# Kernel tuning notes

Hardware: AMD Instinct MI355X
Metric: run time of the kernel (lower is better)

The kernel has to match this reference:

```python
import jax, jax.numpy as jnp
import numpy as np

B, S, D = 8, 2048, 1024
E, K = 16, 2
H = 4096
SD, SH = D // E, H // E  # 64, 256
MAX_SEQ = 2048


def setup_inputs() -> dict:
    key = jax.random.key(0)
    ks = jax.random.split(key, 5)
    x = jax.random.normal(ks[0], (B, S, D), dtype=jnp.float32)
    w_switch = jax.random.normal(ks[1], (D * MAX_SEQ, E), dtype=jnp.float32) * 0.001
    b_switch = jnp.zeros((E,), dtype=jnp.float32)
    w1 = jax.random.normal(ks[2], (E, SD, SH), dtype=jnp.float32) * (1.0 / np.sqrt(SD))
    b1 = jnp.zeros((E, SH), dtype=jnp.float32)
    w2 = jax.random.normal(ks[3], (H, D), dtype=jnp.float32) * (1.0 / np.sqrt(H))
    b2 = jnp.zeros((D,), dtype=jnp.float32)
    return {"x": x, "w_switch": w_switch, "b_switch": b_switch,
            "w1": w1, "b1": b1, "w2": w2, "b2": b2}


def reference(x, w_switch, b_switch, w1, b1, w2, b2):
    # Router: softmax over experts from flattened first MAX_SEQ tokens
    x0 = x[:, :MAX_SEQ].reshape(B, -1)                      # [B, D*MAX_SEQ]
    route_prob = jax.nn.softmax(x0 @ w_switch + b_switch)   # [B, E]
    # Top-k expert membership mask per batch element
    _, topk_idx = jax.lax.top_k(route_prob, K)              # [B, K]
    mask = jax.nn.one_hot(topk_idx, E, dtype=x.dtype).sum(axis=1)  # [B, E]
    # Per-expert linear on the expert's channel slice, masked combine
    xe = x.reshape(B, S, E, SD)                              # [B, S, E, SD]
    h = jnp.einsum('bsed,edh->bseh', xe, w1) + b1            # [B, S, E, SH]
    h = h * mask[:, None, :, None]                           # zero out non-routed
    out = h.reshape(B, S, H)                                 # [B, S, H]
    out = jax.nn.gelu(out, approximate=False)                # exact GELU (torch default)
    return out @ w2 + b2                                     # [B, S, D]
```

## Files before the change

kernel.cpp:

```cpp
#include <hip/hip_runtime.h>
#include <hip/hip_bf16.h>

#define B_  8
#define S_  2048
#define D_  1024
#define E_  16
#define SD_ 64
#define SH_ 256
#define H_  4096
#define R_  (D_ * S_)
#define NBLK_ 2048

typedef __attribute__((ext_vector_type(8))) short bf16x8;
typedef __attribute__((ext_vector_type(4))) float f32x4;

static __device__ __forceinline__ short f2bf(float f) {
    union { float f; unsigned u; } v; v.f = f;
    unsigned r = v.u + 0x7fffu + ((v.u >> 16) & 1u);
    return (short)(r >> 16);
}

__global__ void convert_w(const float* __restrict__ w1, const float* __restrict__ w2,
                          short* __restrict__ w1f, short* __restrict__ w2f) {
    int blk = blockIdx.x;
    if (blk < 128) {
        int t = blk * 256 + threadIdx.x;
        int lane = t & 63, ntile = (t >> 6) & 15, ks = (t >> 10) & 1, e = t >> 11;
        int k0 = ks * 32 + ((lane >> 4) << 3);
        int n  = (ntile << 4) + (lane & 15);
        const float* src = w1 + ((size_t)(e * 64 + k0) * 256 + n);
        bf16x8 o;
        #pragma unroll
        for (int j = 0; j < 8; ++j) o[j] = f2bf(src[(size_t)j * 256]);
        *(bf16x8*)(w1f + ((size_t)t << 3)) = o;
    } else {
        int t = (blk - 128) * 256 + threadIdx.x;
        int lane = t & 63, ntile = (t >> 6) & 63, kg = t >> 12;
        int k0 = (kg << 5) + ((lane >> 4) << 3);
        int n  = (ntile << 4) + (lane & 15);
        const float* src = w2 + ((size_t)k0 * 1024 + n);
        bf16x8 o;
        #pragma unroll
        for (int j = 0; j < 8; ++j) o[j] = f2bf(src[(size_t)j * 1024]);
        *(bf16x8*)(w2f + ((size_t)t << 3)) = o;
    }
}

__global__ __launch_bounds__(256, 4) void router_kernel(const float* __restrict__ x,
                                                        const float* __restrict__ wsw,
                                                        float* __restrict__ partials) {
    __shared__ float red[512];
    int tid = threadIdx.x;
    int wid = tid >> 6, lane = tid & 63;
    int q = lane & 3, rsub = lane >> 2;
    int gw = (blockIdx.x << 2) + wid;
    size_t rowbase = (size_t)gw << 8;
    const float4* w4 = (const float4*)wsw;

    float acc[8][4];
    #pragma unroll
    for (int b = 0; b < 8; ++b)
        #pragma unroll
        for (int j = 0; j < 4; ++j) acc[b][j] = 0.f;

    #pragma unroll 4
    for (int it = 0; it < 16; ++it) {
        size_t row0 = rowbase + (size_t)(it << 4);
        float4 w = w4[row0 * 4 + lane];
        size_t xrow = row0 + rsub;
        float xv[8];
        #pragma unroll
        for (int b = 0; b < 8; ++b) xv[b] = x[(size_t)b * R_ + xrow];
        #pragma unroll
        for (int b = 0; b < 8; ++b) {
            acc[b][0] = fmaf(xv[b], w.x, acc[b][0]);
            acc[b][1] = fmaf(xv[b], w.y, acc[b][1]);
            acc[b][2] = fmaf(xv[b], w.z, acc[b][2]);
            acc[b][3] = fmaf(xv[b], w.w, acc[b][3]);
        }
    }

    #pragma unroll
    for (int b = 0; b < 8; ++b)
        #pragma unroll
        for (int j = 0; j < 4; ++j) {
            float v = acc[b][j];
            v += __shfl_xor(v, 4);
            v += __shfl_xor(v, 8);
            v += __shfl_xor(v, 16);
            v += __shfl_xor(v, 32);
            acc[b][j] = v;
        }

    if (lane < 4) {
        #pragma unroll
        for (int b = 0; b < 8; ++b)
            #pragma unroll
            for (int j = 0; j < 4; ++j)
                red[(wid << 7) + b * 16 + q * 4 + j] = acc[b][j];
    }
    __syncthreads();
    if (tid < 128)
        partials[(size_t)tid * NBLK_ + blockIdx.x] =
            red[tid] + red[128 + tid] + red[256 + tid] + red[384 + tid];
}

__global__ __launch_bounds__(256) void reduce_kernel(const float* __restrict__ partials,
                                                     float* __restrict__ logits) {
    __shared__ float s[256];
    int e = blockIdx.x, tid = threadIdx.x;
    const float4* p4 = (const float4*)(partials + (size_t)e * NBLK_);
    float t = 0.f;
    #pragma unroll
    for (int i = 0; i < 2; ++i) {
        float4 v = p4[i * 256 + tid];
        t += v.x + v.y + v.z + v.w;
    }
    s[tid] = t;
    __syncthreads();
    #pragma unroll
    for (int off = 128; off; off >>= 1) {
        if (tid < off) s[tid] += s[tid + off];
        __syncthreads();
    }
    if (tid == 0) logits[e] = s[0];
}

__global__ void topk_kernel(const float* __restrict__ logits,
                            const float* __restrict__ bsw,
                            int* __restrict__ experts) {
    int b = threadIdx.x;
    if (b >= 8) return;
    float v[16];
    #pragma unroll
    for (int e = 0; e < 16; ++e) v[e] = logits[b * 16 + e] + bsw[e];
    int i0 = 0; float m0 = v[0];
    #pragma unroll
    for (int e = 1; e < 16; ++e) if (v[e] > m0) { m0 = v[e]; i0 = e; }
    int i1 = -1; float m1 = -3.4e38f;
    #pragma unroll
    for (int e = 0; e < 16; ++e) if (e != i0 && v[e] > m1) { m1 = v[e]; i1 = e; }
    experts[2 * b]     = i0;
    experts[2 * b + 1] = i1;
}

__global__ __launch_bounds__(256, 2) void mlp_kernel(
        const float* __restrict__ x, const int* __restrict__ experts,
        const short* __restrict__ w1f, const float* __restrict__ b1,
        const short* __restrict__ w2f, const float* __restrict__ b2,
        float* __restrict__ out) {
    __shared__ short G[32][520];

    int blk  = blockIdx.x;
    int b    = blk & 7;
    int tok0 = (blk >> 3) << 5;
    int e0 = experts[2 * b], e1 = experts[2 * b + 1];
    int tid = threadIdx.x;
    int wid = tid >> 6, lane = tid & 63;
    int slot  = wid >> 1;
    int ex    = slot ? e1 : e0;
    int nhalf = wid & 1;
    int lrow = lane & 15, lk8 = (lane >> 4) << 3;

    f32x4 acc1[2][8];
    #pragma unroll
    for (int m = 0; m < 2; ++m)
        #pragma unroll
        for (int n = 0; n < 8; ++n) acc1[m][n] = (f32x4){0.f, 0.f, 0.f, 0.f};

    #pragma unroll
    for (int ks = 0; ks < 2; ++ks) {
        bf16x8 a[2];
        #pragma unroll
        for (int m = 0; m < 2; ++m) {
            const float* xp = x + (((size_t)b * S_ + tok0 + m * 16 + lrow) * D_
                                   + ex * 64 + ks * 32 + lk8);
            float4 f0 = *(const float4*)xp;
            float4 f1 = *(const float4*)(xp + 4);
            bf16x8 av;
            av[0] = f2bf(f0.x); av[1] = f2bf(f0.y); av[2] = f2bf(f0.z); av[3] = f2bf(f0.w);
            av[4] = f2bf(f1.x); av[5] = f2bf(f1.y); av[6] = f2bf(f1.z); av[7] = f2bf(f1.w);
            a[m] = av;
        }
        #pragma unroll
        for (int nt = 0; nt < 8; ++nt) {
            int ntg = nhalf * 8 + nt;
            bf16x8 bf = *(const bf16x8*)(w1f + ((((size_t)(ex * 2 + ks) * 16 + ntg) * 64 + lane) << 3));
            acc1[0][nt] = __builtin_amdgcn_mfma_f32_16x16x32_bf16(a[0], bf, acc1[0][nt], 0, 0, 0);
            acc1[1][nt] = __builtin_amdgcn_mfma_f32_16x16x32_bf16(a[1], bf, acc1[1][nt], 0, 0, 0);
        }
    }

    #pragma unroll
    for (int nt = 0; nt < 8; ++nt) {
        int ncol = (nhalf * 8 + nt) * 16 + lrow;
        float bb = b1[ex * 256 + ncol];
        #pragma unroll
        for (int m = 0; m < 2; ++m) {
            int r0 = m * 16 + ((lane >> 4) << 2);
            #pragma unroll
            for (int r = 0; r < 4; ++r) {
                float v = acc1[m][nt][r] + bb;
                v = 0.5f * v * (1.0f + erff(v * 0.70710678118f));
                G[r0 + r][slot * 256 + ncol] = f2bf(v);
            }
        }
    }
    __syncthreads();

    f32x4 acc2[2][16];
    #pragma unroll
    for (int m = 0; m < 2; ++m)
        #pragma unroll
        for (int n = 0; n < 16; ++n) acc2[m][n] = (f32x4){0.f, 0.f, 0.f, 0.f};

    for (int ks = 0; ks < 16; ++ks) {
        int e  = (ks < 8) ? e0 : e1;
        int kg = e * 8 + (ks & 7);
        bf16x8 a0 = *(const bf16x8*)&G[lrow][ks * 32 + lk8];
        bf16x8 a1 = *(const bf16x8*)&G[16 + lrow][ks * 32 + lk8];
        #pragma unroll
        for (int nt = 0; nt < 16; ++nt) {
            int ntg = wid * 16 + nt;
            bf16x8 bf = *(const bf16x8*)(w2f + ((((size_t)kg * 64 + ntg) * 64 + lane) << 3));
            acc2[0][nt] = __builtin_amdgcn_mfma_f32_16x16x32_bf16(a0, bf, acc2[0][nt], 0, 0, 0);
            acc2[1][nt] = __builtin_amdgcn_mfma_f32_16x16x32_bf16(a1, bf, acc2[1][nt], 0, 0, 0);
        }
    }

    size_t obase = ((size_t)b * S_ + tok0) * D_;
    #pragma unroll
    for (int nt = 0; nt < 16; ++nt) {
        int d = wid * 256 + nt * 16 + lrow;
        float bb = b2[d];
        #pragma unroll
        for (int m = 0; m < 2; ++m) {
            int r0 = m * 16 + ((lane >> 4) << 2);
            #pragma unroll
            for (int r = 0; r < 4; ++r)
                out[obase + (size_t)(r0 + r) * D_ + d] = acc2[m][nt][r] + bb;
        }
    }
}

extern "C" void kernel_launch(void* const* d_in, const int* in_sizes, int n_in,
                              void* d_out, int out_size, void* d_ws, size_t ws_size,
                              hipStream_t stream) {
    const float* x   = (const float*)d_in[0];
    const float* wsw = (const float*)d_in[1];
    const float* bsw = (const float*)d_in[2];
    const float* w1  = (const float*)d_in[3];
    const float* b1  = (const float*)d_in[4];
    const float* w2  = (const float*)d_in[5];
    const float* b2  = (const float*)d_in[6];
    float* out = (float*)d_out;

    int*   experts  = (int*)d_ws;
    float* logits   = (float*)((char*)d_ws + 512);
    float* partials = (float*)((char*)d_ws + 4096);
    short* w1f = (short*)((char*)d_ws + 4096 + 1048576);
    short* w2f = (short*)((char*)d_ws + 4096 + 1048576 + 524288);

    router_kernel<<<NBLK_, 256, 0, stream>>>(x, wsw, partials);
    reduce_kernel<<<128, 256, 0, stream>>>(partials, logits);
    topk_kernel<<<1, 64, 0, stream>>>(logits, bsw, experts);
    convert_w<<<2176, 256, 0, stream>>>(w1, w2, w1f, w2f);
    mlp_kernel<<<512, 256, 0, stream>>>(x, experts, w1f, b1, w2f, b2, out);
}
```

Baseline: 124.6 us.

## Remap router lanes to batch-by-row and broadcast weights via shuffles

The router GEMV now assigns each lane a batch index and a pair of adjacent rows. x is read as float2 per lane instead of eight scattered scalar loads per lane, and each thread keeps 16 expert accumulators. Weight rows are still loaded once per wave as float4 and broadcast to the lanes that need them through __shfl. This should make the x loads contiguous and cut the reduction shuffles from four levels to three. The cost is 16 shuffles per row pair added to the inner loop.

```diff
diff --git a/kernel.cpp b/kernel.cpp
--- a/kernel.cpp
+++ b/kernel.cpp
@@ -52,52 +52,54 @@
     __shared__ float red[512];
     int tid = threadIdx.x;
     int wid = tid >> 6, lane = tid & 63;
-    int q = lane & 3, rsub = lane >> 2;
+    int b = lane & 7, rh = lane >> 3;
     int gw = (blockIdx.x << 2) + wid;
     size_t rowbase = (size_t)gw << 8;
     const float4* w4 = (const float4*)wsw;
-
-    float acc[8][4];
-    #pragma unroll
-    for (int b = 0; b < 8; ++b)
-        #pragma unroll
-        for (int j = 0; j < 4; ++j) acc[b][j] = 0.f;
-
-    #pragma unroll 4
+    const float2* x2 = (const float2*)(x + (size_t)b * R_ + rowbase) + rh;
+
+    float acc[16];
+    #pragma unroll
+    for (int e = 0; e < 16; ++e) acc[e] = 0.f;
+
+    int sbase = rh << 3;
+
+    #pragma unroll 2
     for (int it = 0; it < 16; ++it) {
-        size_t row0 = rowbase + (size_t)(it << 4);
-        float4 w = w4[row0 * 4 + lane];
-        size_t xrow = row0 + rsub;
-        float xv[8];
-        #pragma unroll
-        for (int b = 0; b < 8; ++b) xv[b] = x[(size_t)b * R_ + xrow];
-        #pragma unroll
-        for (int b = 0; b < 8; ++b) {
-            acc[b][0] = fmaf(xv[b], w.x, acc[b][0]);
-            acc[b][1] = fmaf(xv[b], w.y, acc[b][1]);
-            acc[b][2] = fmaf(xv[b], w.z, acc[b][2]);
-            acc[b][3] = fmaf(xv[b], w.w, acc[b][3]);
-        }
-    }
-
-    #pragma unroll
-    for (int b = 0; b < 8; ++b)
-        #pragma unroll
-        for (int j = 0; j < 4; ++j) {
-            float v = acc[b][j];
-            v += __shfl_xor(v, 4);
-            v += __shfl_xor(v, 8);
-            v += __shfl_xor(v, 16);
-            v += __shfl_xor(v, 32);
-            acc[b][j] = v;
-        }
-
-    if (lane < 4) {
-        #pragma unroll
-        for (int b = 0; b < 8; ++b)
+        float2 xv = x2[it << 3];
+        float4 wA = w4[((rowbase + ((size_t)it << 4)) << 2) + lane];
+
+        #pragma unroll
+        for (int rr = 0; rr < 2; ++rr) {
+            float xs = rr ? xv.y : xv.x;
             #pragma unroll
-            for (int j = 0; j < 4; ++j)
-                red[(wid << 7) + b * 16 + q * 4 + j] = acc[b][j];
+            for (int eq = 0; eq < 4; ++eq) {
+                int s = sbase + (rr << 2) + eq;
+                float w0 = __shfl(wA.x, s);
+                float w1 = __shfl(wA.y, s);
+                float w2v = __shfl(wA.z, s);
+                float w3 = __shfl(wA.w, s);
+                acc[eq * 4 + 0] = fmaf(xs, w0, acc[eq * 4 + 0]);
+                acc[eq * 4 + 1] = fmaf(xs, w1, acc[eq * 4 + 1]);
+                acc[eq * 4 + 2] = fmaf(xs, w2v, acc[eq * 4 + 2]);
+                acc[eq * 4 + 3] = fmaf(xs, w3, acc[eq * 4 + 3]);
+            }
+        }
+    }
+
+    #pragma unroll
+    for (int e = 0; e < 16; ++e) {
+        float v = acc[e];
+        v += __shfl_xor(v, 8);
+        v += __shfl_xor(v, 16);
+        v += __shfl_xor(v, 32);
+        acc[e] = v;
+    }
+
+    if (lane < 8) {
+        #pragma unroll
+        for (int e = 0; e < 16; ++e)
+            red[(wid << 7) + b * 16 + e] = acc[e];
     }
     __syncthreads();
     if (tid < 128)
```

Result: slower. 127.3 us (+2.2%).

## Double-buffer router loads into LDS via async global_load_lds

Applied to the files above, without the earlier changes.

Rewrites the router GEMV so that each block covers 2048 rows in 16 chunks of 128. Each chunk's router weights and x values are staged into double-buffered shared memory with direct global-to-LDS loads, so the next chunk's loads overlap the current chunk's FMAs. The block count is halved, which shrinks the partials buffer, simplifies the reduce kernel and moves the workspace offsets. The intent is better memory coalescing and latency hiding for the bandwidth-bound router. In exchange the kernel adds a barrier per chunk, uses more LDS and runs fewer blocks.

```diff
diff --git a/kernel.cpp b/kernel.cpp
--- a/kernel.cpp
+++ b/kernel.cpp
@@ -9,7 +9,10 @@
 #define SH_ 256
 #define H_  4096
 #define R_  (D_ * S_)
-#define NBLK_ 2048
+#define NBLK_ 1024
+#define RT_ROWS 2048
+#define RT_CHUNK 128
+#define RT_NCHUNK 16
 
 typedef __attribute__((ext_vector_type(8))) short bf16x8;
 typedef __attribute__((ext_vector_type(4))) float f32x4;
@@ -18,6 +21,13 @@
     union { float f; unsigned u; } v; v.f = f;
     unsigned r = v.u + 0x7fffu + ((v.u >> 16) & 1u);
     return (short)(r >> 16);
+}
+
+static __device__ __forceinline__ void gload16(const float* g, float* l) {
+    __builtin_amdgcn_global_load_lds(
+        (const __attribute__((address_space(1))) void*)g,
+        (__attribute__((address_space(3))) void*)l,
+        16, 0, 0);
 }
 
 __global__ void convert_w(const float* __restrict__ w1, const float* __restrict__ w2,
@@ -49,13 +59,31 @@
 __global__ __launch_bounds__(256, 4) void router_kernel(const float* __restrict__ x,
                                                         const float* __restrict__ wsw,
                                                         float* __restrict__ partials) {
+    __shared__ float lw[2][RT_CHUNK * 16];
+    __shared__ float lx[2][8 * RT_CHUNK];
     __shared__ float red[512];
+
     int tid = threadIdx.x;
     int wid = tid >> 6, lane = tid & 63;
-    int q = lane & 3, rsub = lane >> 2;
-    int gw = (blockIdx.x << 2) + wid;
-    size_t rowbase = (size_t)gw << 8;
-    const float4* w4 = (const float4*)wsw;
+    int q = lane & 3, rh = lane >> 2;
+    size_t base = (size_t)blockIdx.x * RT_ROWS;
+
+    #define STAGE(BUF, CHUNK)                                                   \
+        {   size_t cb = base + (size_t)(CHUNK) * RT_CHUNK;                      \
+            _Pragma("unroll")                                                   \
+            for (int k = 0; k < 3; ++k) {                                       \
+                int s = wid * 3 + k;                                            \
+                if (s < 8) {                                                    \
+                    gload16(wsw + (cb + s * 16) * 16 + lane * 4,                \
+                            &lw[BUF][s * 256]);                                 \
+                } else {                                                        \
+                    int s2 = s - 8;                                             \
+                    int b = 2 * s2 + (lane >> 5);                               \
+                    gload16(x + (size_t)b * R_ + cb + (size_t)(lane & 31) * 4,  \
+                            &lx[BUF][s2 * 256]);                                \
+                }                                                               \
+            }                                                                   \
+        }
 
     float acc[8][4];
     #pragma unroll
@@ -63,22 +91,29 @@
         #pragma unroll
         for (int j = 0; j < 4; ++j) acc[b][j] = 0.f;
 
-    #pragma unroll 4
-    for (int it = 0; it < 16; ++it) {
-        size_t row0 = rowbase + (size_t)(it << 4);
-        float4 w = w4[row0 * 4 + lane];
-        size_t xrow = row0 + rsub;
-        float xv[8];
-        #pragma unroll
-        for (int b = 0; b < 8; ++b) xv[b] = x[(size_t)b * R_ + xrow];
-        #pragma unroll
-        for (int b = 0; b < 8; ++b) {
-            acc[b][0] = fmaf(xv[b], w.x, acc[b][0]);
-            acc[b][1] = fmaf(xv[b], w.y, acc[b][1]);
-            acc[b][2] = fmaf(xv[b], w.z, acc[b][2]);
-            acc[b][3] = fmaf(xv[b], w.w, acc[b][3]);
-        }
-    }
+    STAGE(0, 0)
+    __syncthreads();
+
+    for (int c = 0; c < RT_NCHUNK; ++c) {
+        int cur = c & 1;
+        if (c + 1 < RT_NCHUNK) STAGE(cur ^ 1, c + 1)
+
+        #pragma unroll
+        for (int half = 0; half < 2; ++half) {
+            int r = (wid << 5) + (half << 4) + rh;
+            float4 w = *(const float4*)&lw[cur][r * 16 + q * 4];
+            #pragma unroll
+            for (int b = 0; b < 8; ++b) {
+                float xv = lx[cur][b * RT_CHUNK + r];
+                acc[b][0] = fmaf(xv, w.x, acc[b][0]);
+                acc[b][1] = fmaf(xv, w.y, acc[b][1]);
+                acc[b][2] = fmaf(xv, w.z, acc[b][2]);
+                acc[b][3] = fmaf(xv, w.w, acc[b][3]);
+            }
+        }
+        __syncthreads();
+    }
+    #undef STAGE
 
     #pragma unroll
     for (int b = 0; b < 8; ++b)
@@ -110,13 +145,8 @@
     __shared__ float s[256];
     int e = blockIdx.x, tid = threadIdx.x;
     const float4* p4 = (const float4*)(partials + (size_t)e * NBLK_);
-    float t = 0.f;
-    #pragma unroll
-    for (int i = 0; i < 2; ++i) {
-        float4 v = p4[i * 256 + tid];
-        t += v.x + v.y + v.z + v.w;
-    }
-    s[tid] = t;
+    float4 v = p4[tid];
+    s[tid] = v.x + v.y + v.z + v.w;
     __syncthreads();
     #pragma unroll
     for (int off = 128; off; off >>= 1) {
@@ -258,8 +288,8 @@
     int*   experts  = (int*)d_ws;
     float* logits   = (float*)((char*)d_ws + 512);
     float* partials = (float*)((char*)d_ws + 4096);
-    short* w1f = (short*)((char*)d_ws + 4096 + 1048576);
-    short* w2f = (short*)((char*)d_ws + 4096 + 1048576 + 524288);
+    short* w1f = (short*)((char*)d_ws + 4096 + 524288);
+    short* w2f = (short*)((char*)d_ws + 4096 + 524288 + 524288);
 
     router_kernel<<<NBLK_, 256, 0, stream>>>(x, wsw, partials);
     reduce_kernel<<<128, 256, 0, stream>>>(partials, logits);
```

Measured after the change: 110.4 us. 11.4% less time.
